# Kernel optimization log

Hardware: AMD Instinct MI355X
Metric: run time of the kernel (lower is better)

## Reference

```python
import jax, jax.numpy as jnp
import numpy as np

TOP_K = 2  # k in TopKGate


def setup_inputs() -> dict:
    key = jax.random.key(0)
    k1, k2, k3 = jax.random.split(key, 3)
    B, S, H, E = 4, 2048, 1024, 8
    hidden_states = jax.random.normal(k1, (B, S, H), dtype=jnp.float32)
    Wg = jax.random.normal(k2, (H, E), dtype=jnp.float32) * (H ** -0.5)
    We = jax.random.normal(k3, (E, H, H), dtype=jnp.float32) * (H ** -0.5)
    be = jnp.zeros((E, H), dtype=jnp.float32)
    return {"hidden_states": hidden_states, "Wg": Wg, "We": We, "be": be}


def reference(hidden_states, Wg, We, be):
    # hidden_states: [B, S, H]; Wg: [H, E]; We: [E, H, H]; be: [E, H]
    B, S, H = hidden_states.shape
    T = B * S
    x = hidden_states.reshape(T, H)

    # TopKGate: linear gate -> softmax -> top-k -> renormalize combine weights
    probs = jax.nn.softmax(x @ Wg, axis=-1)              # [T, E]
    top_vals, top_idx = jax.lax.top_k(probs, TOP_K)     # [T, K]
    gates = top_vals / jnp.sum(top_vals, axis=-1, keepdims=True)

    # Experts: run each token through each expert Linear, then gather top-k
    expert_out = jnp.einsum('th,ehd->etd', x, We) + be[:, None, :]  # [E, T, H]
    tok = jnp.arange(T)[:, None]                         # [T, 1]
    sel = expert_out[top_idx, tok, :]                    # [T, K, H]

    # Weighted combine over top-k experts
    out = jnp.sum(gates[..., None] * sel, axis=1)        # [T, H]
    return out.reshape(B, S, H)
```

## Files before the change

### kernel.cpp

```cpp
#include <hip/hip_runtime.h>
#include <hip/hip_bf16.h>

#define H 1024
#define NEXP 8
#define T_TOK 8192
#define CAP 8192
#define TM 128
#define TN 128
#define TPB 16
#define CNTSTRIDE 32

typedef __bf16 bf16x8 __attribute__((ext_vector_type(8)));
typedef __bf16 bf16x4 __attribute__((ext_vector_type(4)));
typedef float f32x4 __attribute__((ext_vector_type(4)));

__device__ __forceinline__ void async16(void* lds, const void* g) {
    __builtin_amdgcn_global_load_lds(
        (const __attribute__((address_space(1))) void*)g,
        (__attribute__((address_space(3))) void*)lds, 16, 0, 0);
}

__global__ __launch_bounds__(256) void moe_route(
    const float* __restrict__ x, const float* __restrict__ Wg,
    __bf16* __restrict__ Xb, int* __restrict__ cnt,
    int* __restrict__ ltok, float* __restrict__ lgate,
    int* __restrict__ tsel, float* __restrict__ tgate) {
    const int tid  = threadIdx.x;
    const int lane = tid & 63;
    const int wave = tid >> 6;
    const int base = blockIdx.x * TPB;

    __shared__ int   sE[TPB * 2];
    __shared__ float sG[TPB * 2];
    __shared__ int   lcnt[NEXP], lbase[NEXP], lslot[TPB * 2];

    for (int i = 0; i < TPB / 4; ++i) {
        const int tl = wave * (TPB / 4) + i;
        const int t  = base + tl;
        const float* xr  = x  + (size_t)t * H;
        __bf16*      xbr = Xb + (size_t)t * H;
        float a[NEXP];
#pragma unroll
        for (int e = 0; e < NEXP; ++e) a[e] = 0.f;
#pragma unroll
        for (int j = 0; j < H / 256; ++j) {
            const int h = j * 256 + lane * 4;
            const float4 xv = *(const float4*)(xr + h);
            bf16x4 xo;
            xo[0] = (__bf16)xv.x; xo[1] = (__bf16)xv.y;
            xo[2] = (__bf16)xv.z; xo[3] = (__bf16)xv.w;
            *(bf16x4*)(xbr + h) = xo;
            const float xc[4] = {xv.x, xv.y, xv.z, xv.w};
#pragma unroll
            for (int c = 0; c < 4; ++c) {
                const float4 w0 = *(const float4*)(Wg + (h + c) * NEXP);
                const float4 w1 = *(const float4*)(Wg + (h + c) * NEXP + 4);
                a[0] += xc[c] * w0.x; a[1] += xc[c] * w0.y; a[2] += xc[c] * w0.z; a[3] += xc[c] * w0.w;
                a[4] += xc[c] * w1.x; a[5] += xc[c] * w1.y; a[6] += xc[c] * w1.z; a[7] += xc[c] * w1.w;
            }
        }
#pragma unroll
        for (int e = 0; e < NEXP; ++e) {
#pragma unroll
            for (int off = 32; off > 0; off >>= 1)
                a[e] += __shfl_xor(a[e], off, 64);
        }
        int i0 = 0;
#pragma unroll
        for (int e = 1; e < NEXP; ++e) if (a[e] > a[i0]) i0 = e;
        int i1 = (i0 == 0) ? 1 : 0;
#pragma unroll
        for (int e = 0; e < NEXP; ++e) if (e != i0 && a[e] > a[i1]) i1 = e;
        const float ex = __expf(a[i1] - a[i0]);
        const float g0 = 1.f / (1.f + ex);
        const float g1 = ex / (1.f + ex);
        if (lane == 0) {
            sE[tl * 2] = i0; sE[tl * 2 + 1] = i1;
            sG[tl * 2] = g0; sG[tl * 2 + 1] = g1;
        }
    }
    if (tid < NEXP) lcnt[tid] = 0;
    __syncthreads();
    if (tid < TPB * 2) lslot[tid] = atomicAdd(&lcnt[sE[tid]], 1);
    __syncthreads();
    if (tid < NEXP) lbase[tid] = lcnt[tid] ? atomicAdd(&cnt[tid * CNTSTRIDE], lcnt[tid]) : 0;
    __syncthreads();
    if (tid < TPB * 2) {
        const int e = sE[tid];
        const int s = lbase[e] + lslot[tid];
        const int t = base + (tid >> 1);
        ltok[e * CAP + s]  = t;
        lgate[e * CAP + s] = sG[tid];
        tsel[t * 2 + (tid & 1)]  = e * CAP + s;
        tgate[t * 2 + (tid & 1)] = sG[tid];
    }
}

__global__ __launch_bounds__(256) void cast_transpose_we(
    const float* __restrict__ We, __bf16* __restrict__ WeT) {
    __shared__ float t[64][65];
    const int e  = blockIdx.z;
    const int d0 = blockIdx.x * 64;
    const int h0 = blockIdx.y * 64;
    const int tx = threadIdx.x & 15;
    const int ty = threadIdx.x >> 4;
    const float* src = We + ((size_t)e << 20);
    __bf16* dst = WeT + ((size_t)e << 20);
#pragma unroll
    for (int p = 0; p < 4; ++p) {
        const int row = p * 16 + ty;
        const float4 v = *(const float4*)(src + (size_t)(h0 + row) * H + d0 + tx * 4);
        t[row][tx * 4 + 0] = v.x; t[row][tx * 4 + 1] = v.y;
        t[row][tx * 4 + 2] = v.z; t[row][tx * 4 + 3] = v.w;
    }
    __syncthreads();
#pragma unroll
    for (int p = 0; p < 4; ++p) {
        const int drow = p * 16 + ty;
        bf16x4 o;
        o[0] = (__bf16)t[tx * 4 + 0][drow];
        o[1] = (__bf16)t[tx * 4 + 1][drow];
        o[2] = (__bf16)t[tx * 4 + 2][drow];
        o[3] = (__bf16)t[tx * 4 + 3][drow];
        *(bf16x4*)(dst + (size_t)(d0 + drow) * H + h0 + tx * 4) = o;
    }
}

__global__ __launch_bounds__(256) void moe_gemm(
    const __bf16* __restrict__ Xb, const __bf16* __restrict__ WeT,
    const float* __restrict__ be, const int* __restrict__ cnt,
    const int* __restrict__ ltok, const float* __restrict__ lgate,
    __bf16* __restrict__ Eout) {
    const int e = blockIdx.z;
    const int ne = cnt[e * CNTSTRIDE];
    const int m0 = blockIdx.y * TM;
    if (m0 >= ne) return;
    const int n0 = blockIdx.x * TN;
    int off = 0;
    for (int i2 = 0; i2 < e; ++i2) off += cnt[i2 * CNTSTRIDE];

    __shared__ __align__(16) __bf16 smem[4 * 4096];
    __bf16* Al  = smem;
    __bf16* Al2 = smem + 4096;
    __bf16* Bl  = smem + 8192;
    __bf16* Bl2 = smem + 12288;
    __shared__ int tokL[TM];

    const int tid = threadIdx.x;
    const int lane = tid & 63;
    const int wave = tid >> 6;

    if (tid < TM) {
        const int gi = m0 + tid;
        tokL[tid] = (gi < ne) ? ltok[e * CAP + gi] : 0;
    }
    __syncthreads();

    const __bf16* Bt = WeT + ((size_t)e << 20);
    const int qr = lane >> 4;
    const int rr = lane & 15;
    const int wr = (wave >> 1) * 64;
    const int wc = (wave & 1) * 64;

    f32x4 acc[4][4];
    const f32x4 z = {0.f, 0.f, 0.f, 0.f};
#pragma unroll
    for (int i = 0; i < 4; ++i)
#pragma unroll
        for (int j = 0; j < 4; ++j) acc[i][j] = z;

    const int c0 = tid, c1 = tid + 256;
    const int ar0 = c0 >> 2, ak0 = (((c0 & 3) ^ ((c0 >> 3) & 3)) * 8);
    const int ar1 = c1 >> 2, ak1 = (((c1 & 3) ^ ((c1 >> 3) & 3)) * 8);
    const size_t arow0 = (size_t)tokL[ar0] * H;
    const size_t arow1 = (size_t)tokL[ar1] * H;
    const size_t brow0 = (size_t)(n0 + ar0) * H;
    const size_t brow1 = (size_t)(n0 + ar1) * H;

    for (int k0 = 0; k0 < H; k0 += 64) {
        async16(&Al [c0 * 8], Xb + arow0 + k0 + ak0);
        async16(&Al [c1 * 8], Xb + arow1 + k0 + ak1);
        async16(&Al2[c0 * 8], Xb + arow0 + k0 + 32 + ak0);
        async16(&Al2[c1 * 8], Xb + arow1 + k0 + 32 + ak1);
        async16(&Bl [c0 * 8], Bt + brow0 + k0 + ak0);
        async16(&Bl [c1 * 8], Bt + brow1 + k0 + ak1);
        async16(&Bl2[c0 * 8], Bt + brow0 + k0 + 32 + ak0);
        async16(&Bl2[c1 * 8], Bt + brow1 + k0 + 32 + ak1);
        __syncthreads();
        {
            bf16x8 af[4], bfr[4];
#pragma unroll
            for (int i = 0; i < 4; ++i) {
                const int ra = wr + i * 16 + rr;
                af[i] = *(const bf16x8*)&Al[ra * 32 + ((qr ^ ((ra >> 1) & 3)) * 8)];
            }
#pragma unroll
            for (int j = 0; j < 4; ++j) {
                const int rb = wc + j * 16 + rr;
                bfr[j] = *(const bf16x8*)&Bl[rb * 32 + ((qr ^ ((rb >> 1) & 3)) * 8)];
            }
#pragma unroll
            for (int i = 0; i < 4; ++i)
#pragma unroll
                for (int j = 0; j < 4; ++j)
                    acc[i][j] = __builtin_amdgcn_mfma_f32_16x16x32_bf16(af[i], bfr[j], acc[i][j], 0, 0, 0);
        }
        {
            bf16x8 af[4], bfr[4];
#pragma unroll
            for (int i = 0; i < 4; ++i) {
                const int ra = wr + i * 16 + rr;
                af[i] = *(const bf16x8*)&Al2[ra * 32 + ((qr ^ ((ra >> 1) & 3)) * 8)];
            }
#pragma unroll
            for (int j = 0; j < 4; ++j) {
                const int rb = wc + j * 16 + rr;
                bfr[j] = *(const bf16x8*)&Bl2[rb * 32 + ((qr ^ ((rb >> 1) & 3)) * 8)];
            }
#pragma unroll
            for (int i = 0; i < 4; ++i)
#pragma unroll
                for (int j = 0; j < 4; ++j)
                    acc[i][j] = __builtin_amdgcn_mfma_f32_16x16x32_bf16(af[i], bfr[j], acc[i][j], 0, 0, 0);
        }
        __syncthreads();
    }

    float bev[4];
#pragma unroll
    for (int j = 0; j < 4; ++j) bev[j] = be[e * H + n0 + wc + j * 16 + rr];

    __bf16* Cw = smem + wave * 4096;
#pragma unroll
    for (int i = 0; i < 4; ++i) {
#pragma unroll
        for (int reg = 0; reg < 4; ++reg) {
            const int row = i * 16 + qr * 4 + reg;
            const int key = (row & 7) * 8;
#pragma unroll
            for (int j = 0; j < 4; ++j) {
                const int c = j * 16 + rr;
                Cw[row * 64 + (c ^ key)] = (__bf16)(acc[i][j][reg] + bev[j]);
            }
        }
    }
    const int lrr = lane & 7, lrg = lane >> 3;
#pragma unroll
    for (int p = 0; p < 8; ++p) {
        const int row = p * 8 + lrg;
        const int rglob = m0 + wr + row;
        if (rglob < ne) {
            const int idx8 = ((lrr ^ (row & 7)) * 8);
            const bf16x8 v = *(const bf16x8*)&Cw[row * 64 + idx8];
            *(bf16x8*)(Eout + (size_t)(off + rglob) * H + n0 + wc + lrr * 8) = v;
        }
    }
}

__global__ __launch_bounds__(256) void moe_combine(
    const __bf16* __restrict__ Eout, const int* __restrict__ cnt,
    const int* __restrict__ tsel, const float* __restrict__ tgate,
    float* __restrict__ out) {
    __shared__ int offs[NEXP];
    if (threadIdx.x < NEXP) {
        int o = 0;
        for (int i = 0; i < (int)threadIdx.x; ++i) o += cnt[i * CNTSTRIDE];
        offs[threadIdx.x] = o;
    }
    __syncthreads();
    const int wave = threadIdx.x >> 6, lane = threadIdx.x & 63;
    const int t = blockIdx.x * 4 + wave;
    const int sel0 = tsel[t * 2],  sel1 = tsel[t * 2 + 1];
    const float g0 = tgate[t * 2], g1  = tgate[t * 2 + 1];
    const int e0 = sel0 >> 13, s0 = sel0 & (CAP - 1);
    const int e1 = sel1 >> 13, s1 = sel1 & (CAP - 1);
    const __bf16* r0 = Eout + (size_t)(offs[e0] + s0) * H;
    const __bf16* r1 = Eout + (size_t)(offs[e1] + s1) * H;
    float* orow = out + (size_t)t * H;
#pragma unroll
    for (int c = 0; c < 4; ++c) {
        const int d = c * 256 + lane * 4;
        const bf16x4 a = *(const bf16x4*)(r0 + d);
        const bf16x4 b = *(const bf16x4*)(r1 + d);
        float4 o;
        o.x = g0 * (float)a[0] + g1 * (float)b[0];
        o.y = g0 * (float)a[1] + g1 * (float)b[1];
        o.z = g0 * (float)a[2] + g1 * (float)b[2];
        o.w = g0 * (float)a[3] + g1 * (float)b[3];
        *(float4*)(orow + d) = o;
    }
}

extern "C" void kernel_launch(void* const* d_in, const int* in_sizes, int n_in,
                              void* d_out, int out_size, void* d_ws, size_t ws_size,
                              hipStream_t stream) {
    const float* x  = (const float*)d_in[0];
    const float* Wg = (const float*)d_in[1];
    const float* We = (const float*)d_in[2];
    const float* be = (const float*)d_in[3];
    float* out = (float*)d_out;

    char* ws = (char*)d_ws;
    __bf16* Xb   = (__bf16*)ws;
    __bf16* WeT  = (__bf16*)(ws + ((size_t)16 << 20));
    __bf16* Eout = (__bf16*)(ws + ((size_t)32 << 20));
    char*   meta = ws + ((size_t)64 << 20);
    int*    cnt  = (int*)meta;
    int*    ltok = (int*)(meta + 1024);
    float*  lgat = (float*)(meta + 1024 + (size_t)NEXP * CAP * 4);
    int*    tsel = (int*)(meta + 1024 + (size_t)NEXP * CAP * 8);
    float*  tgat = (float*)(meta + 1024 + (size_t)NEXP * CAP * 8 + (size_t)T_TOK * 8);

    hipMemsetAsync(cnt, 0, NEXP * CNTSTRIDE * sizeof(int), stream);

    cast_transpose_we<<<dim3(H / 64, H / 64, NEXP), 256, 0, stream>>>(We, WeT);
    moe_route<<<T_TOK / TPB, 256, 0, stream>>>(x, Wg, Xb, cnt, ltok, lgat, tsel, tgat);
    moe_gemm<<<dim3(H / TN, T_TOK / TM, NEXP), 256, 0, stream>>>(Xb, WeT, be, cnt, ltok, lgat, Eout);
    moe_combine<<<T_TOK / 4, 256, 0, stream>>>(Eout, cnt, tsel, tgat, out);
}
```

Measured before the change: 198.0 us.

## Fuse weight cast-transpose with routing kernel and flatten GEMM grid ordering

Merges the expert-weight cast/transpose and the gating/routing kernels into one launch, with block ranges dispatching to each role and shared memory aliased between them. This removes one kernel launch and lets the two independent prep phases run concurrently instead of back to back. The GEMM grid is also flattened to 1D with the expert index varying fastest, then the N tile, then the M tile. Blocks for all experts are therefore interleaved, and empty M tiles exit early, spread across the dispatch order rather than bunched at the end. This may change L2 reuse of the weight tiles.

```diff
diff --git a/kernel.cpp b/kernel.cpp
--- a/kernel.cpp
+++ b/kernel.cpp
@@ -9,6 +9,7 @@
 #define TN 128
 #define TPB 16
 #define CNTSTRIDE 32
+#define NTRANS 2048
 
 typedef __bf16 bf16x8 __attribute__((ext_vector_type(8)));
 typedef __bf16 bf16x4 __attribute__((ext_vector_type(4)));
@@ -20,19 +21,54 @@
         (__attribute__((address_space(3))) void*)lds, 16, 0, 0);
 }
 
-__global__ __launch_bounds__(256) void moe_route(
+__global__ __launch_bounds__(256) void moe_prep(
+    const float* __restrict__ We, __bf16* __restrict__ WeT,
     const float* __restrict__ x, const float* __restrict__ Wg,
     __bf16* __restrict__ Xb, int* __restrict__ cnt,
     int* __restrict__ ltok, float* __restrict__ lgate,
     int* __restrict__ tsel, float* __restrict__ tgate) {
-    const int tid  = threadIdx.x;
+    __shared__ __align__(16) char smem[64 * 65 * 4];
+    const int tid = threadIdx.x;
+
+    if (blockIdx.x < NTRANS) {
+        float (*t)[65] = (float(*)[65])smem;
+        const int tt = blockIdx.x;
+        const int e  = tt >> 8;
+        const int d0 = ((tt >> 4) & 15) * 64;
+        const int h0 = (tt & 15) * 64;
+        const int tx = tid & 15;
+        const int ty = tid >> 4;
+        const float* src = We + ((size_t)e << 20);
+        __bf16* dst = WeT + ((size_t)e << 20);
+#pragma unroll
+        for (int p = 0; p < 4; ++p) {
+            const int row = p * 16 + ty;
+            const float4 v = *(const float4*)(src + (size_t)(h0 + row) * H + d0 + tx * 4);
+            t[row][tx * 4 + 0] = v.x; t[row][tx * 4 + 1] = v.y;
+            t[row][tx * 4 + 2] = v.z; t[row][tx * 4 + 3] = v.w;
+        }
+        __syncthreads();
+#pragma unroll
+        for (int p = 0; p < 4; ++p) {
+            const int drow = p * 16 + ty;
+            bf16x4 o;
+            o[0] = (__bf16)t[tx * 4 + 0][drow];
+            o[1] = (__bf16)t[tx * 4 + 1][drow];
+            o[2] = (__bf16)t[tx * 4 + 2][drow];
+            o[3] = (__bf16)t[tx * 4 + 3][drow];
+            *(bf16x4*)(dst + (size_t)(d0 + drow) * H + h0 + tx * 4) = o;
+        }
+        return;
+    }
+
+    int*   sE    = (int*)smem;
+    float* sG    = (float*)(smem + 128);
+    int*   lcnt  = (int*)(smem + 256);
+    int*   lbase = (int*)(smem + 288);
+    int*   lslot = (int*)(smem + 320);
     const int lane = tid & 63;
     const int wave = tid >> 6;
-    const int base = blockIdx.x * TPB;
-
-    __shared__ int   sE[TPB * 2];
-    __shared__ float sG[TPB * 2];
-    __shared__ int   lcnt[NEXP], lbase[NEXP], lslot[TPB * 2];
+    const int base = (blockIdx.x - NTRANS) * TPB;
 
     for (int i = 0; i < TPB / 4; ++i) {
         const int tl = wave * (TPB / 4) + i;
@@ -96,46 +132,18 @@
     }
 }
 
-__global__ __launch_bounds__(256) void cast_transpose_we(
-    const float* __restrict__ We, __bf16* __restrict__ WeT) {
-    __shared__ float t[64][65];
-    const int e  = blockIdx.z;
-    const int d0 = blockIdx.x * 64;
-    const int h0 = blockIdx.y * 64;
-    const int tx = threadIdx.x & 15;
-    const int ty = threadIdx.x >> 4;
-    const float* src = We + ((size_t)e << 20);
-    __bf16* dst = WeT + ((size_t)e << 20);
-#pragma unroll
-    for (int p = 0; p < 4; ++p) {
-        const int row = p * 16 + ty;
-        const float4 v = *(const float4*)(src + (size_t)(h0 + row) * H + d0 + tx * 4);
-        t[row][tx * 4 + 0] = v.x; t[row][tx * 4 + 1] = v.y;
-        t[row][tx * 4 + 2] = v.z; t[row][tx * 4 + 3] = v.w;
-    }
-    __syncthreads();
-#pragma unroll
-    for (int p = 0; p < 4; ++p) {
-        const int drow = p * 16 + ty;
-        bf16x4 o;
-        o[0] = (__bf16)t[tx * 4 + 0][drow];
-        o[1] = (__bf16)t[tx * 4 + 1][drow];
-        o[2] = (__bf16)t[tx * 4 + 2][drow];
-        o[3] = (__bf16)t[tx * 4 + 3][drow];
-        *(bf16x4*)(dst + (size_t)(d0 + drow) * H + h0 + tx * 4) = o;
-    }
-}
-
 __global__ __launch_bounds__(256) void moe_gemm(
     const __bf16* __restrict__ Xb, const __bf16* __restrict__ WeT,
     const float* __restrict__ be, const int* __restrict__ cnt,
     const int* __restrict__ ltok, const float* __restrict__ lgate,
     __bf16* __restrict__ Eout) {
-    const int e = blockIdx.z;
+    const int e  = blockIdx.x & 7;
+    const int nt = (blockIdx.x >> 3) & 7;
+    const int mt = blockIdx.x >> 6;
     const int ne = cnt[e * CNTSTRIDE];
-    const int m0 = blockIdx.y * TM;
+    const int m0 = mt * TM;
     if (m0 >= ne) return;
-    const int n0 = blockIdx.x * TN;
+    const int n0 = nt * TN;
     int off = 0;
     for (int i2 = 0; i2 < e; ++i2) off += cnt[i2 * CNTSTRIDE];
 
@@ -313,8 +321,8 @@
 
     hipMemsetAsync(cnt, 0, NEXP * CNTSTRIDE * sizeof(int), stream);
 
-    cast_transpose_we<<<dim3(H / 64, H / 64, NEXP), 256, 0, stream>>>(We, WeT);
-    moe_route<<<T_TOK / TPB, 256, 0, stream>>>(x, Wg, Xb, cnt, ltok, lgat, tsel, tgat);
-    moe_gemm<<<dim3(H / TN, T_TOK / TM, NEXP), 256, 0, stream>>>(Xb, WeT, be, cnt, ltok, lgat, Eout);
+    moe_prep<<<NTRANS + T_TOK / TPB, 256, 0, stream>>>(We, WeT, x, Wg, Xb, cnt,
+                                                       ltok, lgat, tsel, tgat);
+    moe_gemm<<<8 * 8 * (T_TOK / TM), 256, 0, stream>>>(Xb, WeT, be, cnt, ltok, lgat, Eout);
     moe_combine<<<T_TOK / 4, 256, 0, stream>>>(Eout, cnt, tsel, tgat, out);
 }
```

After: 191.2 us. 3.4% less time.
